# Kernel optimization log

Hardware: AMD Instinct MI355X
Metric: run time of the kernel (lower is better)

Reference implementation:

```python
import jax, jax.numpy as jnp
import numpy as np

SEMA_DIM = 1024
L1, L2, B = 256, 320, 64


def setup_inputs() -> dict:
    key = jax.random.key(0)
    k1, k2, kw1, kb1, kw2, kb2 = jax.random.split(key, 6)
    D = SEMA_DIM
    s = 1.0 / np.sqrt(D)
    return {
        "r1": jax.random.normal(k1, (L1, B, D), dtype=jnp.float32),
        "r2": jax.random.normal(k2, (L2, B, D), dtype=jnp.float32),
        "W1": jax.random.uniform(kw1, (D, D), jnp.float32, -s, s),
        "b1": jax.random.uniform(kb1, (D,), jnp.float32, -s, s),
        "W2": jax.random.uniform(kw2, (D, D), jnp.float32, -s, s),
        "b2": jax.random.uniform(kb2, (D,), jnp.float32, -s, s),
    }


def _mlp(x, W1, b1, W2, b2):
    # torch Linear: x @ W.T + b
    h = jax.nn.relu(x @ W1.T + b1)
    return h @ W2.T + b2


def reference(r1, r2, W1, b1, W2, b2):
    # (L, B, D) -> mlp -> (B, L, D)
    r1 = jnp.transpose(_mlp(r1, W1, b1, W2, b2), (1, 0, 2))  # [B, L1, D]
    r2 = jnp.transpose(_mlp(r2, W1, b1, W2, b2), (1, 0, 2))  # [B, L2, D]

    o = jnp.einsum("bid,bjd->bij", r1, r2)  # [B, L1, L2]
    o1 = jax.nn.softmax(o, axis=2)           # attend r1 -> r2
    o2 = jax.nn.softmax(o, axis=1)           # attend r2 -> r1

    r1_c = jnp.einsum("bij,bjd->bid", o1, r2)  # [B, L1, D]
    r2_c = jnp.einsum("bij,bid->bjd", o2, r1)  # [B, L2, D]

    r1_pool = jnp.concatenate([r1, r1_c], axis=-1).sum(axis=1) / r1.shape[1]  # [B, 2D]
    r2_pool = jnp.concatenate([r2, r2_c], axis=-1).sum(axis=1) / r2.shape[1]  # [B, 2D]
    return (r1_pool, r2_pool)
```

## Files before the change

### kernel.cpp

```cpp
#include <hip/hip_runtime.h>
#include <stdint.h>

#define L1C 256
#define L2C 320
#define BC  64
#define DC  1024

typedef __bf16 bf16_t;
typedef __bf16 bf16x8 __attribute__((ext_vector_type(8)));
typedef __bf16 bf16x4 __attribute__((ext_vector_type(4)));
typedef float  f32x4  __attribute__((ext_vector_type(4)));

__device__ __forceinline__ void gload16(const void* g, void* l) {
  __builtin_amdgcn_global_load_lds(
      (__attribute__((address_space(1))) void*)g,
      (__attribute__((address_space(3))) void*)l, 16, 0, 0);
}

__global__ __launch_bounds__(256)
void conv_kernel(const float* __restrict__ src, bf16_t* __restrict__ dst, int n4) {
  int i = blockIdx.x * 256 + threadIdx.x;
  const int stride = gridDim.x * 256;
  for (; i < n4; i += stride) {
    float4 v = ((const float4*)src)[i];
    bf16x4 o = { (__bf16)v.x, (__bf16)v.y, (__bf16)v.z, (__bf16)v.w };
    ((bf16x4*)dst)[i] = o;
  }
}

__global__ __launch_bounds__(256)
void w2t_kernel(const float* __restrict__ W2, bf16_t* __restrict__ W2T) {
  __shared__ float tile[32][33];
  const int tx = threadIdx.x & 31, ty = threadIdx.x >> 5;
  const int x0 = blockIdx.x * 32, y0 = blockIdx.y * 32;
#pragma unroll
  for (int k = 0; k < 32; k += 8)
    tile[ty + k][tx] = W2[(size_t)(y0 + ty + k) * 1024 + x0 + tx];
  __syncthreads();
#pragma unroll
  for (int k = 0; k < 32; k += 8)
    W2T[(size_t)(x0 + ty + k) * 1024 + y0 + tx] = (bf16_t)tile[tx][ty + k];
}

__global__ __launch_bounds__(256)
void wb_kernel(const float* __restrict__ W2, const float* __restrict__ b2,
               float* __restrict__ w2b) {
  const int dt = threadIdx.x & 15, kg = threadIdx.x >> 4;
  const int d = blockIdx.x * 16 + dt;
  float s = 0.f;
  for (int k = kg * 64; k < kg * 64 + 64; ++k)
    s += W2[(size_t)k * 1024 + d] * b2[k];
  __shared__ float red[16][17];
  red[kg][dt] = s;
  __syncthreads();
  if (kg == 0) {
    float t = 0.f;
#pragma unroll
    for (int g = 0; g < 16; ++g) t += red[g][dt];
    w2b[d] = t;
  }
}

__global__ __launch_bounds__(512, 2)
void mlp_gemm_f32a(const float* __restrict__ R1, const float* __restrict__ R2,
                   const bf16_t* __restrict__ W, const float* __restrict__ bias,
                   bf16_t* __restrict__ C, int Mtiles) {
  const int nwg = Mtiles * 4;
  const int cpx = nwg >> 3;
  const int wg  = ((int)blockIdx.x & 7) * cpx + ((int)blockIdx.x >> 3);
  const int mt = wg >> 2, nt = wg & 3;

  __shared__ __align__(16) char lds[147456];

  const int t    = threadIdx.x;
  const int lane = t & 63, wid = t >> 6;
  const int wm = wid >> 2, wn = wid & 3;
  const int rsel = lane & 15, hi = lane >> 4;
  const int t16 = t * 16;

  const int rT = t >> 3;
  const int gT = (t & 7) ^ (rT & 7);
  const float* Abase = (mt < 64) ? (R1 + (size_t)mt * 256 * 1024)
                                 : (R2 + (size_t)(mt - 64) * 256 * 1024);
  const float* pA[4];
#pragma unroll
  for (int l = 0; l < 4; ++l)
    pA[l] = Abase + (size_t)(l * 64 + rT) * 1024 + gT * 4;

  const int P0 = t16, P1 = 8192 + t16;
  const int Lg0 = P0 ^ ((P0 >> 3) & 0x30);
  const int Lg1 = P1 ^ ((P1 >> 3) & 0x30);
  const bf16_t* pB0 = W + (size_t)(nt * 256 + (Lg0 >> 6)) * 1024 + ((Lg0 & 63) >> 1);
  const bf16_t* pB1 = W + (size_t)(nt * 256 + (Lg1 >> 6)) * 1024 + ((Lg1 & 63) >> 1);

  const int rowA = wm * 128 + rsel;
  const int offA0 = (rowA << 7) + (((2 * hi)     ^ (rsel & 7)) << 4);
  const int offA1 = (rowA << 7) + (((2 * hi + 1) ^ (rsel & 7)) << 4);
  const int kchunk = (hi ^ ((rsel >> 1) & 3)) << 4;
  const int offB = 32768 + ((wn * 64 + rsel) << 6) + kchunk;

  f32x4 acc[8][4] = {};
  bf16x8 bfr[4];

#pragma unroll
  for (int p = 0; p < 2; ++p) {
    char* db = lds + p * 49152;
#pragma unroll
    for (int l = 0; l < 4; ++l) gload16(pA[l] + p * 32, db + l * 8192 + t16);
    gload16(pB0 + p * 32, db + 32768 + t16);
    gload16(pB1 + p * 32, db + 40960 + t16);
  }
  asm volatile("s_waitcnt vmcnt(6)" ::: "memory");
  __builtin_amdgcn_s_barrier();
  __builtin_amdgcn_sched_barrier(0);

  int cur = 0;
#pragma unroll 1
  for (int tt = 0; tt < 32; ++tt) {
    const char* rb = lds + cur * 49152;
    int nx = cur + 2; if (nx >= 3) nx -= 3;
    char* sb = lds + nx * 49152;
    const int ks = (tt + 2) * 32;
    bf16x8 af[4];
#pragma unroll
    for (int m = 0; m < 4; ++m) {
      f32x4 a0 = *(const f32x4*)(rb + offA0 + m * 2048);
      f32x4 a1 = *(const f32x4*)(rb + offA1 + m * 2048);
      af[m] = bf16x8{ (bf16_t)a0[0], (bf16_t)a0[1], (bf16_t)a0[2], (bf16_t)a0[3],
                      (bf16_t)a1[0], (bf16_t)a1[1], (bf16_t)a1[2], (bf16_t)a1[3] };
    }
#pragma unroll
    for (int n = 0; n < 4; ++n) bfr[n] = *(const bf16x8*)(rb + offB + n * 1024);
    if (tt < 30) {
#pragma unroll
      for (int l = 0; l < 4; ++l) gload16(pA[l] + ks, sb + l * 8192 + t16);
    }
    __builtin_amdgcn_s_setprio(1);
#pragma unroll
    for (int m = 0; m < 4; ++m)
#pragma unroll
      for (int n = 0; n < 4; ++n)
        acc[m][n] = __builtin_amdgcn_mfma_f32_16x16x32_bf16(af[m], bfr[n], acc[m][n], 0, 0, 0);
    __builtin_amdgcn_s_setprio(0);
    __builtin_amdgcn_s_barrier();
    __builtin_amdgcn_sched_barrier(0);
#pragma unroll
    for (int m = 0; m < 4; ++m) {
      f32x4 a0 = *(const f32x4*)(rb + offA0 + (m + 4) * 2048);
      f32x4 a1 = *(const f32x4*)(rb + offA1 + (m + 4) * 2048);
      af[m] = bf16x8{ (bf16_t)a0[0], (bf16_t)a0[1], (bf16_t)a0[2], (bf16_t)a0[3],
                      (bf16_t)a1[0], (bf16_t)a1[1], (bf16_t)a1[2], (bf16_t)a1[3] };
    }
    if (tt < 30) {
      gload16(pB0 + ks, sb + 32768 + t16);
      gload16(pB1 + ks, sb + 40960 + t16);
    }
    __builtin_amdgcn_s_setprio(1);
#pragma unroll
    for (int m = 0; m < 4; ++m)
#pragma unroll
      for (int n = 0; n < 4; ++n)
        acc[m + 4][n] = __builtin_amdgcn_mfma_f32_16x16x32_bf16(af[m], bfr[n], acc[m + 4][n], 0, 0, 0);
    __builtin_amdgcn_s_setprio(0);
    if (tt < 30)       asm volatile("s_waitcnt vmcnt(6)" ::: "memory");
    else if (tt == 30) asm volatile("s_waitcnt vmcnt(0)" ::: "memory");
    __builtin_amdgcn_s_barrier();
    __builtin_amdgcn_sched_barrier(0);
    cur = (cur + 1 == 3) ? 0 : cur + 1;
  }

  const int row0 = mt * 256 + wm * 128 + hi * 4;
  const int col0 = nt * 256 + wn * 64 + rsel;
  float bv[4];
#pragma unroll
  for (int n = 0; n < 4; ++n) bv[n] = bias[col0 + n * 16];
#pragma unroll
  for (int m = 0; m < 8; ++m) {
#pragma unroll
    for (int q = 0; q < 4; ++q) {
      const size_t rr = (size_t)(row0 + m * 16 + q) * 1024;
#pragma unroll
      for (int n = 0; n < 4; ++n) {
        float v = fmaxf(acc[m][n][q] + bv[n], 0.f);
        C[rr + col0 + n * 16] = (bf16_t)v;
      }
    }
  }
}

__global__ __launch_bounds__(512, 2)
void mlp_gemm8(const bf16_t* __restrict__ A, const bf16_t* __restrict__ W,
               const float* __restrict__ bias, bf16_t* __restrict__ C,
               int Mtiles, int relu) {
  const int nwg = Mtiles * 4;
  const int cpx = nwg >> 3;
  const int wg  = ((int)blockIdx.x & 7) * cpx + ((int)blockIdx.x >> 3);
  const int mt = wg >> 2, nt = wg & 3;

  __shared__ __align__(16) char lds[131072];

  const int t    = threadIdx.x;
  const int lane = t & 63, wid = t >> 6;
  const int wm = wid >> 2, wn = wid & 3;
  const int rsel = lane & 15, hi = lane >> 4;
  const int t16 = t * 16;

  const int P0 = t16, P1 = 8192 + t16;
  const int Lg0 = P0 ^ ((P0 >> 3) & 0x30);
  const int Lg1 = P1 ^ ((P1 >> 3) & 0x30);
  const int rS0 = Lg0 >> 6, cS0 = (Lg0 & 63) >> 1;
  const int rS1 = Lg1 >> 6, cS1 = (Lg1 & 63) >> 1;
  const bf16_t* pA0 = A + (size_t)(mt * 256 + rS0) * 1024 + cS0;
  const bf16_t* pA1 = A + (size_t)(mt * 256 + rS1) * 1024 + cS1;
  const bf16_t* pB0 = W + (size_t)(nt * 256 + rS0) * 1024 + cS0;
  const bf16_t* pB1 = W + (size_t)(nt * 256 + rS1) * 1024 + cS1;

  const int kchunk = (hi ^ ((rsel >> 1) & 3)) << 4;
  const int offA = ((wm * 128 + rsel) << 6) + kchunk;
  const int offB = 16384 + ((wn * 64 + rsel) << 6) + kchunk;

  f32x4 acc[8][4] = {};
  bf16x8 bfr[4];

#pragma unroll
  for (int p = 0; p < 3; ++p) {
    char* db = lds + p * 32768;
    gload16(pA0 + p * 32, db + t16);
    gload16(pA1 + p * 32, db + 8192 + t16);
    gload16(pB0 + p * 32, db + 16384 + t16);
    gload16(pB1 + p * 32, db + 24576 + t16);
  }
  asm volatile("s_waitcnt vmcnt(8)" ::: "memory");
  __builtin_amdgcn_s_barrier();
  __builtin_amdgcn_sched_barrier(0);

#pragma unroll 1
  for (int tt = 0; tt < 32; ++tt) {
    const char* rb = lds + (tt & 3) * 32768;
    char* sb = lds + ((tt + 3) & 3) * 32768;
    const int ks = (tt + 3) * 32;
    bf16x8 af[4];
#pragma unroll
    for (int m = 0; m < 4; ++m) af[m] = *(const bf16x8*)(rb + offA + m * 1024);
#pragma unroll
    for (int n = 0; n < 4; ++n) bfr[n] = *(const bf16x8*)(rb + offB + n * 1024);
    if (tt < 29) {
      gload16(pA0 + ks, sb + t16);
      gload16(pA1 + ks, sb + 8192 + t16);
    }
    __builtin_amdgcn_s_setprio(1);
#pragma unroll
    for (int m = 0; m < 4; ++m)
#pragma unroll
      for (int n = 0; n < 4; ++n)
        acc[m][n] = __builtin_amdgcn_mfma_f32_16x16x32_bf16(af[m], bfr[n], acc[m][n], 0, 0, 0);
    __builtin_amdgcn_s_setprio(0);
    __builtin_amdgcn_s_barrier();
    __builtin_amdgcn_sched_barrier(0);
#pragma unroll
    for (int m = 0; m < 4; ++m) af[m] = *(const bf16x8*)(rb + offA + (m + 4) * 1024);
    if (tt < 29) {
      gload16(pB0 + ks, sb + 16384 + t16);
      gload16(pB1 + ks, sb + 24576 + t16);
    }
    __builtin_amdgcn_s_setprio(1);
#pragma unroll
    for (int m = 0; m < 4; ++m)
#pragma unroll
      for (int n = 0; n < 4; ++n)
        acc[m + 4][n] = __builtin_amdgcn_mfma_f32_16x16x32_bf16(af[m], bfr[n], acc[m + 4][n], 0, 0, 0);
    __builtin_amdgcn_s_setprio(0);
    if (tt < 29)       asm volatile("s_waitcnt vmcnt(8)" ::: "memory");
    else if (tt == 29) asm volatile("s_waitcnt vmcnt(4)" ::: "memory");
    else if (tt == 30) asm volatile("s_waitcnt vmcnt(0)" ::: "memory");
    __builtin_amdgcn_s_barrier();
    __builtin_amdgcn_sched_barrier(0);
  }

  const int row0 = mt * 256 + wm * 128 + hi * 4;
  const int col0 = nt * 256 + wn * 64 + rsel;
  float bv[4];
#pragma unroll
  for (int n = 0; n < 4; ++n) bv[n] = bias[col0 + n * 16];
#pragma unroll
  for (int m = 0; m < 8; ++m) {
#pragma unroll
    for (int q = 0; q < 4; ++q) {
      const size_t rr = (size_t)(row0 + m * 16 + q) * 1024;
#pragma unroll
      for (int n = 0; n < 4; ++n) {
        float v = acc[m][n][q] + bv[n];
        if (relu) v = fmaxf(v, 0.f);
        C[rr + col0 + n * 16] = (bf16_t)v;
      }
    }
  }
}

__global__ __launch_bounds__(256)
void gemmK(const bf16_t* __restrict__ A, const bf16_t* __restrict__ W,
           float* __restrict__ P, int KS) {
  const int slice = (int)blockIdx.x >> 6;
  const int tl = (int)blockIdx.x & 63;
  const int mt = tl >> 3, nt = tl & 7;
  const int koff = slice * KS;

  const int f = threadIdx.x;
  const int lane = f & 63, w = f >> 6;
  const int sRow = f >> 2, sCol8 = (f & 3) * 8;

  const bf16_t* Ab = A + (size_t)mt * 128 * 1024 + (size_t)sRow * 1024 + sCol8;
  const bf16_t* Bb = W + (size_t)nt * 128 * 1024 + (size_t)sRow * 1024 + sCol8;

  __shared__ __align__(16) bf16_t sA[128 * 32];
  __shared__ __align__(16) bf16_t sB[128 * 32];
  bf16_t* sAp = sA + sRow * 32 + sCol8;
  bf16_t* sBp = sB + sRow * 32 + sCol8;

  const int wr = (w >> 1) * 64, wc = (w & 1) * 64;
  const int rsel = lane & 15, koff2 = (lane >> 4) * 8;
  const bf16_t* rA = sA + (wr + rsel) * 32 + koff2;
  const bf16_t* rB = sB + (wc + rsel) * 32 + koff2;

  f32x4 acc[4][4] = {};
  for (int kt = koff; kt < koff + KS; kt += 32) {
    __syncthreads();
    gload16(Ab + kt,             sAp);
    gload16(Ab + kt + 64 * 1024, sAp + 64 * 32);
    gload16(Bb + kt,             sBp);
    gload16(Bb + kt + 64 * 1024, sBp + 64 * 32);
    asm volatile("s_waitcnt vmcnt(0)" ::: "memory");
    __syncthreads();
    bf16x8 af[4], bfv[4];
#pragma unroll
    for (int m = 0; m < 4; ++m) af[m] = *(const bf16x8*)(rA + m * 16 * 32);
#pragma unroll
    for (int n = 0; n < 4; ++n) bfv[n] = *(const bf16x8*)(rB + n * 16 * 32);
#pragma unroll
    for (int m = 0; m < 4; ++m)
#pragma unroll
      for (int n = 0; n < 4; ++n)
        acc[m][n] = __builtin_amdgcn_mfma_f32_16x16x32_bf16(af[m], bfv[n], acc[m][n], 0, 0, 0);
  }

  float* Pb = P + (size_t)slice * 1048576;
  const int row0 = mt * 128 + wr + (lane >> 4) * 4;
  const int col0 = nt * 128 + wc + rsel;
#pragma unroll
  for (int n = 0; n < 4; ++n) {
    const int c = col0 + n * 16;
#pragma unroll
    for (int m = 0; m < 4; ++m) {
      const int r = row0 + m * 16;
#pragma unroll
      for (int q = 0; q < 4; ++q)
        Pb[(size_t)(r + q) * 1024 + c] = acc[m][n][q];
    }
  }
}

__global__ __launch_bounds__(256)
void g_reduce(const float* __restrict__ Gp, bf16_t* __restrict__ GB) {
  const int i4 = blockIdx.x * 256 + threadIdx.x;
  float4 a = ((const float4*)Gp)[i4];
  float4 b = ((const float4*)(Gp + 1048576))[i4];
  float4 c = ((const float4*)(Gp + 2097152))[i4];
  float4 d = ((const float4*)(Gp + 3145728))[i4];
  bf16x4 o = { (bf16_t)(a.x + b.x + c.x + d.x), (bf16_t)(a.y + b.y + c.y + d.y),
               (bf16_t)(a.z + b.z + c.z + d.z), (bf16_t)(a.w + b.w + c.w + d.w) };
  ((bf16x4*)GB)[i4] = o;
}

__global__ __launch_bounds__(256)
void pool_gemmK(const bf16_t* __restrict__ A, const bf16_t* __restrict__ W,
                float* __restrict__ P) {
  const int slice = (int)blockIdx.x >> 4;
  const int tl = (int)blockIdx.x & 15;
  const int mt = tl >> 3, nt = tl & 7;
  const int koff = slice * 128;

  const int f = threadIdx.x;
  const int lane = f & 63, w = f >> 6;
  const int sRow = f >> 2, sCol8 = (f & 3) * 8;

  const bf16_t* Ab = A + (size_t)mt * 128 * 1024 + (size_t)sRow * 1024 + sCol8;
  const bf16_t* Bb = W + (size_t)nt * 128 * 1024 + (size_t)sRow * 1024 + sCol8;

  __shared__ __align__(16) bf16_t sA[128 * 32];
  __shared__ __align__(16) bf16_t sB[128 * 32];
  bf16_t* sAp = sA + sRow * 32 + sCol8;
  bf16_t* sBp = sB + sRow * 32 + sCol8;

  const int wr = (w >> 1) * 64, wc = (w & 1) * 64;
  const int rsel = lane & 15, koff2 = (lane >> 4) * 8;
  const bf16_t* rA = sA + (wr + rsel) * 32 + koff2;
  const bf16_t* rB = sB + (wc + rsel) * 32 + koff2;

  f32x4 acc[4][4] = {};
  for (int kt = koff; kt < koff + 128; kt += 32) {
    __syncthreads();
    gload16(Ab + kt,             sAp);
    gload16(Ab + kt + 64 * 1024, sAp + 64 * 32);
    gload16(Bb + kt,             sBp);
    gload16(Bb + kt + 64 * 1024, sBp + 64 * 32);
    asm volatile("s_waitcnt vmcnt(0)" ::: "memory");
    __syncthreads();
    bf16x8 af[4], bfv[4];
#pragma unroll
    for (int m = 0; m < 4; ++m) af[m] = *(const bf16x8*)(rA + m * 16 * 32);
#pragma unroll
    for (int n = 0; n < 4; ++n) bfv[n] = *(const bf16x8*)(rB + n * 16 * 32);
#pragma unroll
    for (int m = 0; m < 4; ++m)
#pragma unroll
      for (int n = 0; n < 4; ++n)
        acc[m][n] = __builtin_amdgcn_mfma_f32_16x16x32_bf16(af[m], bfv[n], acc[m][n], 0, 0, 0);
  }

  float* Pb = P + (size_t)slice * 262144;
  const int row0 = mt * 128 + wr + (lane >> 4) * 4;
  const int col0 = nt * 128 + wc + rsel;
#pragma unroll
  for (int n = 0; n < 4; ++n) {
    const int c = col0 + n * 16;
#pragma unroll
    for (int m = 0; m < 4; ++m) {
      const int r = row0 + m * 16;
#pragma unroll
      for (int q = 0; q < 4; ++q)
        Pb[(size_t)(r + q) * 1024 + c] = acc[m][n][q];
    }
  }
}

__global__ __launch_bounds__(256)
void pool_reduce(const float* __restrict__ Pp, const float* __restrict__ b2,
                 float* __restrict__ out) {
  const int idx = blockIdx.x * 256 + threadIdx.x;
  const int r = idx >> 10, c = idx & 1023;
  float s = b2[c];
#pragma unroll
  for (int sl = 0; sl < 8; ++sl) s += Pp[(size_t)sl * 262144 + idx];
  const int g = r >> 6, b = r & 63;
  out[(size_t)(g >> 1) * 131072 + (size_t)b * 2048 + (g & 1) * 1024 + c] = s;
}

__global__ __launch_bounds__(256)
void t_kernel(const bf16_t* __restrict__ H, const float* __restrict__ w2b,
              float* __restrict__ tT1, float* __restrict__ tT2) {
  const int wv = threadIdx.x >> 6, lane = threadIdx.x & 63;
  const int r = blockIdx.x * 4 + wv;
  const bf16_t* hrow = H + (size_t)r * 1024;
  float s = 0.f;
#pragma unroll
  for (int h = 0; h < 2; ++h) {
    bf16x8 v = *(const bf16x8*)(hrow + h * 512 + lane * 8);
#pragma unroll
    for (int e = 0; e < 8; ++e) s += (float)v[e] * w2b[h * 512 + lane * 8 + e];
  }
#pragma unroll
  for (int off = 32; off; off >>= 1) s += __shfl_xor(s, off);
  if (lane == 0) {
    const int b = r & 63;
    if (r < 16384) tT1[b * L1C + (r >> 6)] = s;
    else           tT2[b * L2C + ((r - 16384) >> 6)] = s;
  }
}

__global__ __launch_bounds__(256)
void logits_gemm(const bf16_t* __restrict__ Y1, const bf16_t* __restrict__ Y2,
                 float* __restrict__ O) {
  const int wg = ((int)blockIdx.x & 7) * 48 + ((int)blockIdx.x >> 3);
  const int b = wg / 6, t = wg % 6;
  const int mt = t / 3, nt = t % 3;

  const int f = threadIdx.x;
  const int lane = f & 63, w = f >> 6;
  const int sRow = f >> 2, sCol8 = (f & 3) * 8;

  const int i0 = mt * 128 + sRow;
  const int i1 = i0 + 64;
  int j0 = nt * 128 + sRow;      if (j0 > L2C - 1) j0 = L2C - 1;
  int j1 = nt * 128 + sRow + 64; if (j1 > L2C - 1) j1 = L2C - 1;
  const bf16_t* A0 = Y1 + ((size_t)i0 * BC + b) * DC + sCol8;
  const bf16_t* A1 = Y1 + ((size_t)i1 * BC + b) * DC + sCol8;
  const bf16_t* B0 = Y2 + ((size_t)j0 * BC + b) * DC + sCol8;
  const bf16_t* B1 = Y2 + ((size_t)j1 * BC + b) * DC + sCol8;

  __shared__ __align__(16) bf16_t sA[128 * 32];
  __shared__ __align__(16) bf16_t sB[128 * 32];
  bf16_t* sAp = sA + sRow * 32 + sCol8;
  bf16_t* sBp = sB + sRow * 32 + sCol8;

  const int wr = (w >> 1) * 64, wc = (w & 1) * 64;
  const int rsel = lane & 15, koff = (lane >> 4) * 8;
  const bf16_t* rA = sA + (wr + rsel) * 32 + koff;
  const bf16_t* rB = sB + (wc + rsel) * 32 + koff;

  f32x4 acc[4][4] = {};
  for (int kt = 0; kt < 1024; kt += 32) {
    __syncthreads();
    gload16(A0 + kt, sAp);
    gload16(A1 + kt, sAp + 64 * 32);
    gload16(B0 + kt, sBp);
    gload16(B1 + kt, sBp + 64 * 32);
    asm volatile("s_waitcnt vmcnt(0)" ::: "memory");
    __syncthreads();
    bf16x8 af[4], bfv[4];
#pragma unroll
    for (int m = 0; m < 4; ++m) af[m] = *(const bf16x8*)(rA + m * 16 * 32);
#pragma unroll
    for (int n = 0; n < 4; ++n) bfv[n] = *(const bf16x8*)(rB + n * 16 * 32);
#pragma unroll
    for (int m = 0; m < 4; ++m)
#pragma unroll
      for (int n = 0; n < 4; ++n)
        acc[m][n] = __builtin_amdgcn_mfma_f32_16x16x32_bf16(af[m], bfv[n], acc[m][n], 0, 0, 0);
  }

  float* Ob = O + (size_t)b * L1C * L2C;
  const int row0 = mt * 128 + wr + (lane >> 4) * 4;
  const int col0 = nt * 128 + wc + rsel;
#pragma unroll
  for (int n = 0; n < 4; ++n) {
    const int c = col0 + n * 16;
    if (c < L2C) {
#pragma unroll
      for (int m = 0; m < 4; ++m) {
        const int r = row0 + m * 16;
#pragma unroll
        for (int q = 0; q < 4; ++q)
          Ob[(size_t)(r + q) * L2C + c] = acc[m][n][q];
      }
    }
  }
}

__global__ __launch_bounds__(256)
void row_stats(const float* __restrict__ O, const float* __restrict__ tT2,
               float* __restrict__ rowM, float* __restrict__ rowInv) {
  const int gw = blockIdx.x * 4 + (threadIdx.x >> 6);
  const int lane = threadIdx.x & 63;
  const int b = gw >> 8;
  const float* row = O + (size_t)gw * L2C;
  const float* t2 = tT2 + b * L2C;
  float v[5];
  float m = -1e30f;
#pragma unroll
  for (int t = 0; t < 5; ++t) { v[t] = row[t * 64 + lane] + t2[t * 64 + lane]; m = fmaxf(m, v[t]); }
#pragma unroll
  for (int off = 32; off; off >>= 1) m = fmaxf(m, __shfl_xor(m, off));
  float s = 0.f;
#pragma unroll
  for (int t = 0; t < 5; ++t) s += __expf(v[t] - m);
#pragma unroll
  for (int off = 32; off; off >>= 1) s += __shfl_xor(s, off);
  if (lane == 0) { rowM[gw] = m; rowInv[gw] = 1.f / s; }
}

__global__ __launch_bounds__(256)
void col_stats_c1(const float* __restrict__ O, const float* __restrict__ tT1,
                  const float* __restrict__ tT2,
                  const float* __restrict__ rowM, const float* __restrict__ rowInv,
                  float* __restrict__ colM, float* __restrict__ colInv,
                  float* __restrict__ c1) {
  const int b = blockIdx.x / 5, jb = blockIdx.x % 5;
  const int jl = threadIdx.x & 63, ig = threadIdx.x >> 6;
  const int j = jb * 64 + jl;
  const float* Ob = O + (size_t)b * L1C * L2C + j;
  const float* rM = rowM + b * L1C;
  const float* rI = rowInv + b * L1C;
  const float* t1 = tT1 + b * L1C;
  const float t2j = tT2[b * L2C + j];
  float m = -1e30f, s = 0.f, cp = 0.f;
  for (int i = ig; i < L1C; i += 4) {
    float ov = Ob[(size_t)i * L2C];
    float v = ov + t1[i];
    float mn = fmaxf(m, v);
    s = s * __expf(m - mn) + __expf(v - mn);
    m = mn;
    cp += __expf(ov + t2j - rM[i]) * rI[i];
  }
  __shared__ float sm[4][64], ss[4][64], sc[4][64];
  sm[ig][jl] = m; ss[ig][jl] = s; sc[ig][jl] = cp;
  __syncthreads();
  if (ig == 0) {
    for (int g = 1; g < 4; ++g) {
      float mg = sm[g][jl], sg = ss[g][jl];
      float mn = fmaxf(m, mg);
      s = s * __expf(m - mn) + sg * __expf(mg - mn);
      m = mn;
      cp += sc[g][jl];
    }
    colM[b * L2C + j] = m;
    colInv[b * L2C + j] = 1.f / s;
    c1[b * L2C + j] = cp;
  }
}

__global__ __launch_bounds__(256)
void c2_kernel(const float* __restrict__ O, const float* __restrict__ tT1,
               const float* __restrict__ colM, const float* __restrict__ colInv,
               float* __restrict__ c2) {
  const int gw = blockIdx.x * 4 + (threadIdx.x >> 6);
  const int lane = threadIdx.x & 63;
  const int b = gw >> 8;
  const float* row = O + (size_t)gw * L2C;
  const float* cM = colM + b * L2C;
  const float* cI = colInv + b * L2C;
  const float t1i = tT1[b * L1C + (gw & 255)];
  float s = 0.f;
#pragma unroll
  for (int t = 0; t < 5; ++t) {
    const int j = t * 64 + lane;
    s += __expf(row[j] + t1i - cM[j]) * cI[j];
  }
#pragma unroll
  for (int off = 32; off; off >>= 1) s += __shfl_xor(s, off);
  if (lane == 0) c2[gw] = s;
}

__global__ __launch_bounds__(256)
void u_kernel(const bf16_t* __restrict__ H, const float* __restrict__ c1,
              const float* __restrict__ c2, bf16_t* __restrict__ Ub) {
  const int b = blockIdx.x >> 2;
  const int d = (blockIdx.x & 3) * 256 + threadIdx.x;
  const bf16_t* H2 = H + (size_t)L1C * BC * DC;
  float s1 = 0.f, s1c = 0.f, s2 = 0.f, s2c = 0.f;
  const float* c2b = c2 + b * L1C;
  for (int i = 0; i < L1C; ++i) {
    float v = (float)H[((size_t)i * BC + b) * DC + d];
    s1 += v; s1c += c2b[i] * v;
  }
  const float* c1b = c1 + b * L2C;
  for (int j = 0; j < L2C; ++j) {
    float v = (float)H2[((size_t)j * BC + b) * DC + d];
    s2 += v; s2c += c1b[j] * v;
  }
  Ub[(size_t)(0 * 64 + b) * 1024 + d] = (bf16_t)(s1  * (1.f / L1C));
  Ub[(size_t)(1 * 64 + b) * 1024 + d] = (bf16_t)(s2c * (1.f / L1C));
  Ub[(size_t)(2 * 64 + b) * 1024 + d] = (bf16_t)(s2  * (1.f / L2C));
  Ub[(size_t)(3 * 64 + b) * 1024 + d] = (bf16_t)(s1c * (1.f / L2C));
}

extern "C" void kernel_launch(void* const* d_in, const int* in_sizes, int n_in,
                              void* d_out, int out_size, void* d_ws, size_t ws_size,
                              hipStream_t stream) {
  const float* r1 = (const float*)d_in[0];
  const float* r2 = (const float*)d_in[1];
  const float* W1 = (const float*)d_in[2];
  const float* b1 = (const float*)d_in[3];
  const float* W2 = (const float*)d_in[4];
  const float* b2 = (const float*)d_in[5];
  float* out = (float*)d_out;
  char* ws = (char*)d_ws;

  const size_t M1 = (size_t)L1C * BC;
  const size_t M2 = (size_t)L2C * BC;
  const size_t Mt = M1 + M2;

  size_t off = 0;
  bf16_t* XB  = (bf16_t*)(ws + off); off += Mt * DC * 2;
  bf16_t* HB  = (bf16_t*)(ws + off); off += Mt * DC * 2;
  bf16_t* WB1 = (bf16_t*)(ws + off); off += (size_t)DC * DC * 2;
  bf16_t* WB2 = (bf16_t*)(ws + off); off += (size_t)DC * DC * 2;
  bf16_t* W2T = (bf16_t*)(ws + off); off += (size_t)DC * DC * 2;
  bf16_t* GB  = (bf16_t*)(ws + off); off += (size_t)DC * DC * 2;
  float* w2b   = (float*)(ws + off); off += 4096;
  float* zb    = (float*)(ws + off); off += 4096;
  float* tT1   = (float*)(ws + off); off += BC * L1C * 4;
  float* tT2   = (float*)(ws + off); off += BC * L2C * 4;
  float* rowM  = (float*)(ws + off); off += BC * L1C * 4;
  float* rowIv = (float*)(ws + off); off += BC * L1C * 4;
  float* colM  = (float*)(ws + off); off += BC * L2C * 4;
  float* colIv = (float*)(ws + off); off += BC * L2C * 4;
  float* c1v   = (float*)(ws + off); off += BC * L2C * 4;
  float* c2v   = (float*)(ws + off); off += BC * L1C * 4;
  bf16_t* Ub   = (bf16_t*)(ws + off); off += 256 * DC * 2;

  bf16_t* Z = XB;
  float*  O = (float*)((char*)XB + 35651584);
  float*  Gpart = (float*)((char*)XB + 58720256);
  float*  Ppart = (float*)HB;
  bf16_t* H2 = HB + M1 * DC;

  conv_kernel<<<512, 256, 0, stream>>>(W1, WB1, (int)((size_t)DC * DC / 4));
  conv_kernel<<<512, 256, 0, stream>>>(W2, WB2, (int)((size_t)DC * DC / 4));
  w2t_kernel<<<dim3(32, 32), 256, 0, stream>>>(W2, W2T);
  wb_kernel<<<64, 256, 0, stream>>>(W2, b2, w2b);
  (void)hipMemsetAsync(zb, 0, 4096, stream);

  mlp_gemm_f32a<<<576, 512, 0, stream>>>(r1, r2, WB1, b1, HB, 144);

  gemmK<<<256, 256, 0, stream>>>(W2T, W2T, Gpart, 256);
  t_kernel<<<9216, 256, 0, stream>>>(HB, w2b, tT1, tT2);
  g_reduce<<<1024, 256, 0, stream>>>(Gpart, GB);

  mlp_gemm8<<<256, 512, 0, stream>>>(HB, GB, zb, Z, 64, 0);

  logits_gemm<<<384, 256, 0, stream>>>(Z, H2, O);

  row_stats<<<4096, 256, 0, stream>>>(O, tT2, rowM, rowIv);
  col_stats_c1<<<320, 256, 0, stream>>>(O, tT1, tT2, rowM, rowIv, colM, colIv, c1v);
  c2_kernel<<<4096, 256, 0, stream>>>(O, tT1, colM, colIv, c2v);

  u_kernel<<<256, 256, 0, stream>>>(HB, c1v, c2v, Ub);
  pool_gemmK<<<128, 256, 0, stream>>>(Ub, WB2, Ppart);
  pool_reduce<<<1024, 256, 0, stream>>>(Ppart, b2, out);
}
```

Baseline: 307.0 us.

## Convert A tile to bf16 in registers before LDS store in MLP GEMM

The first MLP GEMM previously streamed fp32 activations straight into LDS with global_load_lds and converted them to bf16 on every fragment read. It now loads the fp32 A tile into registers, converts it once, and writes bf16 to LDS with a new swizzle. This cuts LDS from 144KB to 96KB and halves the A-fragment LDS read traffic. In exchange it adds register pressure and exposes the A global loads through explicit vmcnt waits in the middle of the iteration, which may weaken overlap.

```diff
diff --git a/kernel.cpp b/kernel.cpp
--- a/kernel.cpp
+++ b/kernel.cpp
@@ -15,6 +15,11 @@
   __builtin_amdgcn_global_load_lds(
       (__attribute__((address_space(1))) void*)g,
       (__attribute__((address_space(3))) void*)l, 16, 0, 0);
+}
+
+__device__ __forceinline__ bf16x8 cvt8(f32x4 a, f32x4 b) {
+  return bf16x8{ (bf16_t)a[0], (bf16_t)a[1], (bf16_t)a[2], (bf16_t)a[3],
+                 (bf16_t)b[0], (bf16_t)b[1], (bf16_t)b[2], (bf16_t)b[3] };
 }
 
 __global__ __launch_bounds__(256)
@@ -70,7 +75,7 @@
   const int wg  = ((int)blockIdx.x & 7) * cpx + ((int)blockIdx.x >> 3);
   const int mt = wg >> 2, nt = wg & 3;
 
-  __shared__ __align__(16) char lds[147456];
+  __shared__ __align__(16) char lds[98304];
 
   const int t    = threadIdx.x;
   const int lane = t & 63, wid = t >> 6;
@@ -78,14 +83,12 @@
   const int rsel = lane & 15, hi = lane >> 4;
   const int t16 = t * 16;
 
-  const int rT = t >> 3;
-  const int gT = (t & 7) ^ (rT & 7);
+  const int rW = t >> 2;
+  const int k0 = ((t & 3) ^ ((rW >> 1) & 3)) * 8;
   const float* Abase = (mt < 64) ? (R1 + (size_t)mt * 256 * 1024)
                                  : (R2 + (size_t)(mt - 64) * 256 * 1024);
-  const float* pA[4];
-#pragma unroll
-  for (int l = 0; l < 4; ++l)
-    pA[l] = Abase + (size_t)(l * 64 + rT) * 1024 + gT * 4;
+  const float* pAg0 = Abase + (size_t)rW * 1024 + k0;
+  const float* pAg1 = Abase + (size_t)(rW + 128) * 1024 + k0;
 
   const int P0 = t16, P1 = 8192 + t16;
   const int Lg0 = P0 ^ ((P0 >> 3) & 0x30);
@@ -93,47 +96,55 @@
   const bf16_t* pB0 = W + (size_t)(nt * 256 + (Lg0 >> 6)) * 1024 + ((Lg0 & 63) >> 1);
   const bf16_t* pB1 = W + (size_t)(nt * 256 + (Lg1 >> 6)) * 1024 + ((Lg1 & 63) >> 1);
 
-  const int rowA = wm * 128 + rsel;
-  const int offA0 = (rowA << 7) + (((2 * hi)     ^ (rsel & 7)) << 4);
-  const int offA1 = (rowA << 7) + (((2 * hi + 1) ^ (rsel & 7)) << 4);
   const int kchunk = (hi ^ ((rsel >> 1) & 3)) << 4;
-  const int offB = 32768 + ((wn * 64 + rsel) << 6) + kchunk;
+  const int offA = ((wm * 128 + rsel) << 6) + kchunk;
+  const int offB = 16384 + ((wn * 64 + rsel) << 6) + kchunk;
 
   f32x4 acc[8][4] = {};
   bf16x8 bfr[4];
 
-#pragma unroll
-  for (int p = 0; p < 2; ++p) {
-    char* db = lds + p * 49152;
-#pragma unroll
-    for (int l = 0; l < 4; ++l) gload16(pA[l] + p * 32, db + l * 8192 + t16);
-    gload16(pB0 + p * 32, db + 32768 + t16);
-    gload16(pB1 + p * 32, db + 40960 + t16);
-  }
-  asm volatile("s_waitcnt vmcnt(6)" ::: "memory");
+  {
+    f32x4 a0 = *(const f32x4*)(pAg0);
+    f32x4 a1 = *(const f32x4*)(pAg0 + 4);
+    f32x4 a2 = *(const f32x4*)(pAg1);
+    f32x4 a3 = *(const f32x4*)(pAg1 + 4);
+    f32x4 a4 = *(const f32x4*)(pAg0 + 32);
+    f32x4 a5 = *(const f32x4*)(pAg0 + 36);
+    f32x4 a6 = *(const f32x4*)(pAg1 + 32);
+    f32x4 a7 = *(const f32x4*)(pAg1 + 36);
+    gload16(pB0,      lds + 16384 + t16);
+    gload16(pB1,      lds + 24576 + t16);
+    gload16(pB0 + 32, lds + 32768 + 16384 + t16);
+    gload16(pB1 + 32, lds + 32768 + 24576 + t16);
+    *(bf16x8*)(lds + t16)                = cvt8(a0, a1);
+    *(bf16x8*)(lds + 8192 + t16)         = cvt8(a2, a3);
+    *(bf16x8*)(lds + 32768 + t16)        = cvt8(a4, a5);
+    *(bf16x8*)(lds + 32768 + 8192 + t16) = cvt8(a6, a7);
+  }
+  asm volatile("s_waitcnt vmcnt(0) lgkmcnt(0)" ::: "memory");
   __builtin_amdgcn_s_barrier();
   __builtin_amdgcn_sched_barrier(0);
 
   int cur = 0;
 #pragma unroll 1
   for (int tt = 0; tt < 32; ++tt) {
-    const char* rb = lds + cur * 49152;
+    const char* rb = lds + cur * 32768;
     int nx = cur + 2; if (nx >= 3) nx -= 3;
-    char* sb = lds + nx * 49152;
+    char* sb = lds + nx * 32768;
     const int ks = (tt + 2) * 32;
+    f32x4 L0, L1, L2, L3;
     bf16x8 af[4];
 #pragma unroll
-    for (int m = 0; m < 4; ++m) {
-      f32x4 a0 = *(const f32x4*)(rb + offA0 + m * 2048);
-      f32x4 a1 = *(const f32x4*)(rb + offA1 + m * 2048);
-      af[m] = bf16x8{ (bf16_t)a0[0], (bf16_t)a0[1], (bf16_t)a0[2], (bf16_t)a0[3],
-                      (bf16_t)a1[0], (bf16_t)a1[1], (bf16_t)a1[2], (bf16_t)a1[3] };
-    }
+    for (int m = 0; m < 4; ++m) af[m] = *(const bf16x8*)(rb + offA + m * 1024);
 #pragma unroll
     for (int n = 0; n < 4; ++n) bfr[n] = *(const bf16x8*)(rb + offB + n * 1024);
     if (tt < 30) {
-#pragma unroll
-      for (int l = 0; l < 4; ++l) gload16(pA[l] + ks, sb + l * 8192 + t16);
+      L0 = *(const f32x4*)(pAg0 + ks);
+      L1 = *(const f32x4*)(pAg0 + ks + 4);
+      L2 = *(const f32x4*)(pAg1 + ks);
+      L3 = *(const f32x4*)(pAg1 + ks + 4);
+      gload16(pB0 + ks, sb + 16384 + t16);
+      gload16(pB1 + ks, sb + 24576 + t16);
     }
     __builtin_amdgcn_s_setprio(1);
 #pragma unroll
@@ -145,15 +156,11 @@
     __builtin_amdgcn_s_barrier();
     __builtin_amdgcn_sched_barrier(0);
 #pragma unroll
-    for (int m = 0; m < 4; ++m) {
-      f32x4 a0 = *(const f32x4*)(rb + offA0 + (m + 4) * 2048);
-      f32x4 a1 = *(const f32x4*)(rb + offA1 + (m + 4) * 2048);
-      af[m] = bf16x8{ (bf16_t)a0[0], (bf16_t)a0[1], (bf16_t)a0[2], (bf16_t)a0[3],
-                      (bf16_t)a1[0], (bf16_t)a1[1], (bf16_t)a1[2], (bf16_t)a1[3] };
-    }
+    for (int m = 0; m < 4; ++m) af[m] = *(const bf16x8*)(rb + offA + (m + 4) * 1024);
     if (tt < 30) {
-      gload16(pB0 + ks, sb + 32768 + t16);
-      gload16(pB1 + ks, sb + 40960 + t16);
+      asm volatile("s_waitcnt vmcnt(2)" ::: "memory");
+      *(bf16x8*)(sb + t16)        = cvt8(L0, L1);
+      *(bf16x8*)(sb + 8192 + t16) = cvt8(L2, L3);
     }
     __builtin_amdgcn_s_setprio(1);
 #pragma unroll
@@ -162,8 +169,8 @@
       for (int n = 0; n < 4; ++n)
         acc[m + 4][n] = __builtin_amdgcn_mfma_f32_16x16x32_bf16(af[m], bfr[n], acc[m + 4][n], 0, 0, 0);
     __builtin_amdgcn_s_setprio(0);
-    if (tt < 30)       asm volatile("s_waitcnt vmcnt(6)" ::: "memory");
-    else if (tt == 30) asm volatile("s_waitcnt vmcnt(0)" ::: "memory");
+    if (tt == 30) asm volatile("s_waitcnt vmcnt(0)" ::: "memory");
+    asm volatile("s_waitcnt lgkmcnt(0)" ::: "memory");
     __builtin_amdgcn_s_barrier();
     __builtin_amdgcn_sched_barrier(0);
     cur = (cur + 1 == 3) ? 0 : cur + 1;
```

Result: slower. 348.6 us (+13.5%).

## Fuse w2b dot into first MLP epilogue and pipeline logits GEMM loads

Applied to the files above, without the earlier changes.

Moves the per-row dot product of H with w2b into the epilogue of the first MLP GEMM. Each wave writes a partial sum, and a small t_red kernel reduces the 16 partials, replacing the t_kernel that re-read all of H from memory. Separately, the logits GEMM gets a 4-stage LDS ring buffer with swizzled layout, async global-to-LDS prefetch three tiles ahead, and priority hints, to overlap loads with MFMA. The costs are extra epilogue shuffles, a tpart workspace and more LDS use in the logits kernel.

```diff
diff --git a/kernel.cpp b/kernel.cpp
--- a/kernel.cpp
+++ b/kernel.cpp
@@ -64,7 +64,8 @@
 __global__ __launch_bounds__(512, 2)
 void mlp_gemm_f32a(const float* __restrict__ R1, const float* __restrict__ R2,
                    const bf16_t* __restrict__ W, const float* __restrict__ bias,
-                   bf16_t* __restrict__ C, int Mtiles) {
+                   bf16_t* __restrict__ C, int Mtiles,
+                   const float* __restrict__ w2b, float* __restrict__ tpart) {
   const int nwg = Mtiles * 4;
   const int cpx = nwg >> 3;
   const int wg  = ((int)blockIdx.x & 7) * cpx + ((int)blockIdx.x >> 3);
@@ -185,6 +186,46 @@
         C[rr + col0 + n * 16] = (bf16_t)v;
       }
     }
+  }
+
+  {
+    float wv[4];
+#pragma unroll
+    for (int n = 0; n < 4; ++n) wv[n] = w2b[col0 + n * 16];
+    float* tp = tpart + (size_t)(nt * 4 + wn) * 36864;
+#pragma unroll
+    for (int m = 0; m < 8; ++m) {
+#pragma unroll
+      for (int q = 0; q < 4; ++q) {
+        float s = 0.f;
+#pragma unroll
+        for (int n = 0; n < 4; ++n) {
+          float v = fmaxf(acc[m][n][q] + bv[n], 0.f);
+          v = (float)(bf16_t)v;
+          s += v * wv[n];
+        }
+        s += __shfl_xor(s, 1);
+        s += __shfl_xor(s, 2);
+        s += __shfl_xor(s, 4);
+        s += __shfl_xor(s, 8);
+        if (rsel == 0)
+          tp[row0 + m * 16 + q] = s;
+      }
+    }
+  }
+}
+
+__global__ __launch_bounds__(256)
+void t_red(const float* __restrict__ tp, float* __restrict__ tT1,
+           float* __restrict__ tT2) {
+  const int r = blockIdx.x * 256 + threadIdx.x;
+  float s = 0.f;
+#pragma unroll
+  for (int k = 0; k < 16; ++k) s += tp[(size_t)k * 36864 + r];
+  if (r < 16384) tT1[(r & 63) * L1C + (r >> 6)] = s;
+  else {
+    const int r2 = r - 16384;
+    tT2[(r2 & 63) * L2C + (r2 >> 6)] = s;
   }
 }
 
@@ -446,37 +487,19 @@
 }
 
 __global__ __launch_bounds__(256)
-void t_kernel(const bf16_t* __restrict__ H, const float* __restrict__ w2b,
-              float* __restrict__ tT1, float* __restrict__ tT2) {
-  const int wv = threadIdx.x >> 6, lane = threadIdx.x & 63;
-  const int r = blockIdx.x * 4 + wv;
-  const bf16_t* hrow = H + (size_t)r * 1024;
-  float s = 0.f;
-#pragma unroll
-  for (int h = 0; h < 2; ++h) {
-    bf16x8 v = *(const bf16x8*)(hrow + h * 512 + lane * 8);
-#pragma unroll
-    for (int e = 0; e < 8; ++e) s += (float)v[e] * w2b[h * 512 + lane * 8 + e];
-  }
-#pragma unroll
-  for (int off = 32; off; off >>= 1) s += __shfl_xor(s, off);
-  if (lane == 0) {
-    const int b = r & 63;
-    if (r < 16384) tT1[b * L1C + (r >> 6)] = s;
-    else           tT2[b * L2C + ((r - 16384) >> 6)] = s;
-  }
-}
-
-__global__ __launch_bounds__(256)
 void logits_gemm(const bf16_t* __restrict__ Y1, const bf16_t* __restrict__ Y2,
                  float* __restrict__ O) {
   const int wg = ((int)blockIdx.x & 7) * 48 + ((int)blockIdx.x >> 3);
-  const int b = wg / 6, t = wg % 6;
-  const int mt = t / 3, nt = t % 3;
-
-  const int f = threadIdx.x;
-  const int lane = f & 63, w = f >> 6;
-  const int sRow = f >> 2, sCol8 = (f & 3) * 8;
+  const int b = wg / 6, t6 = wg % 6;
+  const int mt = t6 / 3, nt = t6 % 3;
+
+  __shared__ __align__(16) char lds[65536];
+
+  const int t = threadIdx.x;
+  const int lane = t & 63, w = t >> 6;
+  const int sRow = t >> 2;
+  const int sCol8 = (((t & 3) ^ ((t >> 3) & 3))) * 8;
+  const int t16 = t * 16;
 
   const int i0 = mt * 128 + sRow;
   const int i1 = i0 + 64;
@@ -487,39 +510,58 @@
   const bf16_t* B0 = Y2 + ((size_t)j0 * BC + b) * DC + sCol8;
   const bf16_t* B1 = Y2 + ((size_t)j1 * BC + b) * DC + sCol8;
 
-  __shared__ __align__(16) bf16_t sA[128 * 32];
-  __shared__ __align__(16) bf16_t sB[128 * 32];
-  bf16_t* sAp = sA + sRow * 32 + sCol8;
-  bf16_t* sBp = sB + sRow * 32 + sCol8;
-
   const int wr = (w >> 1) * 64, wc = (w & 1) * 64;
-  const int rsel = lane & 15, koff = (lane >> 4) * 8;
-  const bf16_t* rA = sA + (wr + rsel) * 32 + koff;
-  const bf16_t* rB = sB + (wc + rsel) * 32 + koff;
+  const int rsel = lane & 15, hi = lane >> 4;
+  const int kchunk = (hi ^ ((rsel >> 1) & 3)) << 4;
+  const int offA = ((wr + rsel) << 6) + kchunk;
+  const int offB = 8192 + ((wc + rsel) << 6) + kchunk;
 
   f32x4 acc[4][4] = {};
-  for (int kt = 0; kt < 1024; kt += 32) {
-    __syncthreads();
-    gload16(A0 + kt, sAp);
-    gload16(A1 + kt, sAp + 64 * 32);
-    gload16(B0 + kt, sBp);
-    gload16(B1 + kt, sBp + 64 * 32);
-    asm volatile("s_waitcnt vmcnt(0)" ::: "memory");
-    __syncthreads();
+
+#pragma unroll
+  for (int p = 0; p < 3; ++p) {
+    char* db = lds + p * 16384;
+    gload16(A0 + p * 32, db + t16);
+    gload16(A1 + p * 32, db + 4096 + t16);
+    gload16(B0 + p * 32, db + 8192 + t16);
+    gload16(B1 + p * 32, db + 12288 + t16);
+  }
+  asm volatile("s_waitcnt vmcnt(8)" ::: "memory");
+  __builtin_amdgcn_s_barrier();
+  __builtin_amdgcn_sched_barrier(0);
+
+#pragma unroll 1
+  for (int tt = 0; tt < 32; ++tt) {
+    const char* rb = lds + (tt & 3) * 16384;
+    char* sb = lds + ((tt + 3) & 3) * 16384;
+    const int ks = (tt + 3) * 32;
     bf16x8 af[4], bfv[4];
 #pragma unroll
-    for (int m = 0; m < 4; ++m) af[m] = *(const bf16x8*)(rA + m * 16 * 32);
-#pragma unroll
-    for (int n = 0; n < 4; ++n) bfv[n] = *(const bf16x8*)(rB + n * 16 * 32);
+    for (int m = 0; m < 4; ++m) af[m] = *(const bf16x8*)(rb + offA + m * 1024);
+#pragma unroll
+    for (int n = 0; n < 4; ++n) bfv[n] = *(const bf16x8*)(rb + offB + n * 1024);
+    if (tt < 29) {
+      gload16(A0 + ks, sb + t16);
+      gload16(A1 + ks, sb + 4096 + t16);
+      gload16(B0 + ks, sb + 8192 + t16);
+      gload16(B1 + ks, sb + 12288 + t16);
+    }
+    __builtin_amdgcn_s_setprio(1);
 #pragma unroll
     for (int m = 0; m < 4; ++m)
 #pragma unroll
       for (int n = 0; n < 4; ++n)
         acc[m][n] = __builtin_amdgcn_mfma_f32_16x16x32_bf16(af[m], bfv[n], acc[m][n], 0, 0, 0);
+    __builtin_amdgcn_s_setprio(0);
+    if (tt < 29)       asm volatile("s_waitcnt vmcnt(8)" ::: "memory");
+    else if (tt == 29) asm volatile("s_waitcnt vmcnt(4)" ::: "memory");
+    else if (tt == 30) asm volatile("s_waitcnt vmcnt(0)" ::: "memory");
+    __builtin_amdgcn_s_barrier();
+    __builtin_amdgcn_sched_barrier(0);
   }
 
   float* Ob = O + (size_t)b * L1C * L2C;
-  const int row0 = mt * 128 + wr + (lane >> 4) * 4;
+  const int row0 = mt * 128 + wr + hi * 4;
   const int col0 = nt * 128 + wc + rsel;
 #pragma unroll
   for (int n = 0; n < 4; ++n) {
@@ -677,6 +719,7 @@
   float* c1v   = (float*)(ws + off); off += BC * L2C * 4;
   float* c2v   = (float*)(ws + off); off += BC * L1C * 4;
   bf16_t* Ub   = (bf16_t*)(ws + off); off += 256 * DC * 2;
+  float* tpart = (float*)(ws + off); off += (size_t)16 * Mt * 4;
 
   bf16_t* Z = XB;
   float*  O = (float*)((char*)XB + 35651584);
@@ -690,10 +733,10 @@
   wb_kernel<<<64, 256, 0, stream>>>(W2, b2, w2b);
   (void)hipMemsetAsync(zb, 0, 4096, stream);
 
-  mlp_gemm_f32a<<<576, 512, 0, stream>>>(r1, r2, WB1, b1, HB, 144);
+  mlp_gemm_f32a<<<576, 512, 0, stream>>>(r1, r2, WB1, b1, HB, 144, w2b, tpart);
+  t_red<<<144, 256, 0, stream>>>(tpart, tT1, tT2);
 
   gemmK<<<256, 256, 0, stream>>>(W2T, W2T, Gpart, 256);
-  t_kernel<<<9216, 256, 0, stream>>>(HB, w2b, tT1, tT2);
   g_reduce<<<1024, 256, 0, stream>>>(Gpart, GB);
 
   mlp_gemm8<<<256, 512, 0, stream>>>(HB, GB, zb, Z, 64, 0);
```

Measured after the change: 304.0 us. No clear change (-1.0%).
